# Kernel tuning notes

Hardware: AMD Instinct MI355X
Metric: run time of the kernel (lower is better)

The kernel has to match this reference:

```python
import jax, jax.numpy as jnp
import numpy as np

T, B, E, H = 2048, 4, 1024, 16
EH = E // H  # 64


def setup_inputs() -> dict:
    rng = jax.random.key(0)
    ks = jax.random.split(rng, 8)
    s = 0.02  # weight init scale to keep softmax logits reasonable
    return {
        "query": jax.random.normal(ks[0], (T, B, E), jnp.float32),
        "key": jax.random.normal(ks[1], (T, B, E), jnp.float32),
        "value": jax.random.normal(ks[2], (T, B, E), jnp.float32),
        "mask": jax.random.uniform(ks[3], (T, T), jnp.float32),
        "w_qkv": jax.random.normal(ks[4], (3 * E, E), jnp.float32) * s,
        "b_qkv": jax.random.normal(ks[5], (3 * E,), jnp.float32) * s,
        "w_out": jax.random.normal(ks[6], (E, E), jnp.float32) * s,
        "b_out": jax.random.normal(ks[7], (E,), jnp.float32) * s,
    }


def reference(query, key, value, mask, w_qkv, b_qkv, w_out, b_out):
    # query/key/value: [T, B, E] (sequence-first, as in the torch module)
    t, b, e = query.shape
    eh = e // H
    wq, wk, wv = jnp.split(w_qkv, 3, axis=0)  # each [E, E]
    bq, bk, bv = jnp.split(b_qkv, 3, axis=0)

    def proj_heads(x, w, bias):
        y = x @ w.T + bias                    # [T, B, E]
        # [T,B,H,Eh] -> [B,H,T,Eh]  (matches unflatten/transpose/permute chain)
        return y.reshape(t, b, H, eh).transpose(1, 2, 0, 3)

    q = proj_heads(query, wq, bq)             # [B, H, T, Eh]
    k = proj_heads(key, wk, bk)
    v = proj_heads(value, wv, bv)

    scale = 1.0 / np.sqrt(eh).astype(np.float32)
    scores = jnp.einsum('bhqd,bhkd->bhqk', q, k) * scale   # [B,H,T,T]
    scores = scores * mask[None, None, :, :]               # multiplicative mask
    # is_causal=False, attn_mask=None -> attn_bias is zeros (skip identity add)
    attn = jax.nn.softmax(scores, axis=-1)
    # dropout=0.0 -> identity
    ctx = jnp.einsum('bhqk,bhkd->bhqd', attn, v)           # [B,H,T,Eh]
    ctx = ctx.transpose(0, 2, 1, 3).reshape(b, t, e)       # [B,T,E]
    out = ctx @ w_out.T + b_out                            # [B,T,E]
    return out.transpose(1, 0, 2)                          # [T,B,E]
```

## Files before the change

kernel.cpp:

```cpp
#include <hip/hip_runtime.h>
#include <hip/hip_bf16.h>
#include <stdint.h>

#define T_DIM 2048
#define B_DIM 4
#define E_DIM 1024
#define H_DIM 16
#define EHD 64
#define L2E 1.4426950408889634f
#define QSCALE (0.125f * L2E)
#define FMAXC 12.0f

typedef __attribute__((ext_vector_type(8))) short bf16x8;
typedef __attribute__((ext_vector_type(4))) float f32x4;
typedef __attribute__((ext_vector_type(16))) float f32x16;
typedef __attribute__((ext_vector_type(2))) float f32x2;
typedef __attribute__((ext_vector_type(2))) unsigned u32x2;
typedef __attribute__((ext_vector_type(4))) unsigned u32x4;

__device__ __forceinline__ unsigned short f2bf(float x) {
  unsigned int u = __builtin_bit_cast(unsigned int, x);
  u += 0x7fffu + ((u >> 16) & 1u);
  return (unsigned short)(u >> 16);
}

__device__ __forceinline__ unsigned pkbf(float a, float b) {
  return (unsigned)f2bf(a) | ((unsigned)f2bf(b) << 16);
}

__device__ __forceinline__ unsigned pk_trunc(float a, float b) {
  return (__builtin_bit_cast(unsigned, a) >> 16) |
         (__builtin_bit_cast(unsigned, b) & 0xffff0000u);
}

__device__ __forceinline__ f32x2 bfpair1(unsigned w) {
  u32x2 u = {w << 16, w & 0xffff0000u};
  return __builtin_bit_cast(f32x2, u);
}

__device__ __forceinline__ void gload16(const void* g, void* l) {
  __builtin_amdgcn_global_load_lds(
      (const __attribute__((address_space(1))) void*)g,
      (__attribute__((address_space(3))) void*)l, 16, 0, 0);
}

__global__ __launch_bounds__(256) void cvt_fused(
    const float4* __restrict__ q, const float4* __restrict__ k,
    const float4* __restrict__ v, const float4* __restrict__ wqkv,
    const float4* __restrict__ wout, uint2* __restrict__ xq,
    uint2* __restrict__ xk, uint2* __restrict__ xv, uint2* __restrict__ wq,
    uint2* __restrict__ wo) {
  int i = blockIdx.x * 256 + threadIdx.x;
  const int stride = gridDim.x * 256;
  for (; i < 7340032; i += stride) {
    const float4* s;
    uint2* d;
    int j;
    if (i < 2097152) { s = q; d = xq; j = i; }
    else if (i < 4194304) { s = k; d = xk; j = i - 2097152; }
    else if (i < 6291456) { s = v; d = xv; j = i - 4194304; }
    else if (i < 7077888) { s = wqkv; d = wq; j = i - 6291456; }
    else { s = wout; d = wo; j = i - 7077888; }
    const float4 f = s[j];
    uint2 o;
    o.x = pkbf(f.x, f.y);
    o.y = pkbf(f.z, f.w);
    d[j] = o;
  }
}

__global__ __launch_bounds__(256) void mask_perm(const float* __restrict__ mask,
                                                 uint2* __restrict__ out) {
  const int idx = blockIdx.x * 256 + threadIdx.x;
  const int q = idx >> 8;
  const int k = (idx & 255) * 8;
  const float4 a = *(const float4*)(mask + (size_t)q * T_DIM + k);
  const float4 b = *(const float4*)(mask + (size_t)q * T_DIM + k + 4);
  const int qblk = q >> 7, wave = (q >> 5) & 3, ql = q & 31;
  const int t = k >> 6, kb = (k >> 5) & 1, half = (k >> 4) & 1;
  const int rem8 = (k >> 3) & 1;
  const int cbase = ((((qblk * 32 + t) * 4 + wave) * 2 + kb) * 2 + half) * 64;
  uint2 w0, w1;
  w0.x = pkbf(a.x, a.y);
  w0.y = pkbf(a.z, a.w);
  w1.x = pkbf(b.x, b.y);
  w1.y = pkbf(b.z, b.w);
  out[(size_t)(cbase + ql) * 2 + rem8] = w0;
  out[(size_t)(cbase + 32 + ql) * 2 + rem8] = w1;
}

template <int MODE>
__global__ __launch_bounds__(256) void gemm_kernel(
    const unsigned short* __restrict__ Abase,
    const unsigned short* __restrict__ Bt,
    const float* __restrict__ bias,
    void* __restrict__ outv, int K) {
  __shared__ alignas(16) short As[128 * 32];
  __shared__ alignas(16) short Bs[128 * 32];
  const int tid = threadIdx.x;
  const int lane = tid & 63, wave = tid >> 6;
  const int m0 = blockIdx.x * 128, n0 = blockIdx.y * 128;
  const int wr = wave >> 1, wc = wave & 1;
  const int lrow = lane & 15, lgrp = lane >> 4;

  const unsigned short* A = Abase;
  if (MODE == 0) A += (size_t)(n0 >> 10) * (8192u * 1024u);

  f32x4 acc[4][4];
#pragma unroll
  for (int m = 0; m < 4; ++m)
#pragma unroll
    for (int n = 0; n < 4; ++n) acc[m][n] = (f32x4){0.f, 0.f, 0.f, 0.f};

  const int srow = wave * 16 + (lane >> 2);
  const int scol = (lane & 3) * 8;
  short* lA0 = As + wave * 16 * 32;
  short* lA1 = As + (64 + wave * 16) * 32;
  short* lB0 = Bs + wave * 16 * 32;
  short* lB1 = Bs + (64 + wave * 16) * 32;

  for (int k0 = 0; k0 < K; k0 += 32) {
    const unsigned short* ga = A + (size_t)(m0 + srow) * K + k0 + scol;
    const unsigned short* gb = Bt + (size_t)(n0 + srow) * K + k0 + scol;
    gload16(ga, lA0);
    gload16(ga + (size_t)64 * K, lA1);
    gload16(gb, lB0);
    gload16(gb + (size_t)64 * K, lB1);
    __syncthreads();
    const short* pa = As + (wr * 64 + lrow) * 32 + lgrp * 8;
    const short* pb = Bs + (wc * 64 + lrow) * 32 + lgrp * 8;
    bf16x8 a[4], b[4];
#pragma unroll
    for (int m = 0; m < 4; ++m) a[m] = *(const bf16x8*)(pa + m * 512);
#pragma unroll
    for (int n = 0; n < 4; ++n) b[n] = *(const bf16x8*)(pb + n * 512);
#pragma unroll
    for (int m = 0; m < 4; ++m)
#pragma unroll
      for (int n = 0; n < 4; ++n)
        acc[m][n] = __builtin_amdgcn_mfma_f32_16x16x32_bf16(a[m], b[n], acc[m][n], 0, 0, 0);
    __syncthreads();
  }

#pragma unroll
  for (int n = 0; n < 4; ++n) {
    const int gn = n0 + wc * 64 + n * 16 + lrow;
    const float bv = bias[gn];
    if (MODE == 0) {
      unsigned short* out = (unsigned short*)outv;
      const int which = gn >> 10;
      const float qsc = (which == 0) ? QSCALE : 1.0f;
      const int e = gn & 1023;
      const int hh = e >> 6, dd = e & 63;
#pragma unroll
      for (int m = 0; m < 4; ++m)
#pragma unroll
        for (int r = 0; r < 4; ++r) {
          const int gm = m0 + wr * 64 + m * 16 + lgrp * 4 + r;
          const int t = gm >> 2, bb = gm & 3;
          const unsigned short val = f2bf((acc[m][n][r] + bv) * qsc);
          const size_t rbase = ((size_t)which * 64 + bb * 16 + hh) * 131072;
          if (which == 0) {
            out[rbase + (size_t)t * 64 + dd] = val;
          } else if (which == 1) {
            out[rbase + (t >> 6) * 4096 +
                (((t >> 5) & 1) * 4 + (dd >> 4)) * 512 +
                ((((dd >> 3) & 1) << 5) + (t & 31)) * 8 + (dd & 7)] = val;
          } else {
            out[rbase + (t >> 6) * 4096 +
                ((dd >> 5) * 4 + ((t >> 4) & 3)) * 512 +
                ((((t >> 3) & 1) << 5) + (dd & 31)) * 8 + (t & 7)] = val;
          }
        }
    } else {
      float* out = (float*)outv;
#pragma unroll
      for (int m = 0; m < 4; ++m)
#pragma unroll
        for (int r = 0; r < 4; ++r) {
          const int gm = m0 + wr * 64 + m * 16 + lgrp * 4 + r;
          const int bb = gm >> 11, t = gm & 2047;
          out[((size_t)t * B_DIM + bb) * E_DIM + gn] = acc[m][n][r] + bv;
        }
    }
  }
}

__global__ __launch_bounds__(256, 3) void attn_kernel(
    const unsigned short* __restrict__ Qm, const unsigned short* __restrict__ KPg,
    const unsigned short* __restrict__ VPg, const unsigned short* __restrict__ Mb,
    unsigned short* __restrict__ ctx) {
  __shared__ alignas(16) short Ks[2][4096];
  __shared__ alignas(16) short Vs[2][4096];
  const int tid = threadIdx.x, lane = tid & 63, wave = tid >> 6;
  const int ql = lane & 31, hi = lane >> 5;
  const int bh = blockIdx.y, b = bh >> 4, h = bh & 15;
  const int q0 = blockIdx.x * 128;
  const int qrow = q0 + wave * 32 + ql;

  const size_t base = (size_t)bh * (T_DIM * EHD);
  const uint4* mb4 = (const uint4*)Mb + (size_t)blockIdx.x * 32768 +
                     wave * 256 + lane;

  bf16x8 qf[4];
#pragma unroll
  for (int i = 0; i < 4; ++i)
    qf[i] = *(const bf16x8*)(Qm + base + (size_t)qrow * 64 + i * 16 + hi * 8);

  f32x16 accO0 = {0.f, 0.f, 0.f, 0.f, 0.f, 0.f, 0.f, 0.f,
                  0.f, 0.f, 0.f, 0.f, 0.f, 0.f, 0.f, 0.f};
  f32x16 accO1 = accO0;
  f32x2 racc2 = {0.f, 0.f};

  uint4 mreg[2][4];

#define STAGE(bufi, T_)                                                         \
  {                                                                             \
    _Pragma("unroll") for (int s2 = 0; s2 < 2; ++s2) {                          \
      const int s = wave * 2 + s2;                                              \
      gload16(KPg + base + (size_t)(T_) * 4096 + s * 512 + lane * 8,            \
              &Ks[bufi][s * 512]);                                              \
      gload16(VPg + base + (size_t)(T_) * 4096 + s * 512 + lane * 8,            \
              &Vs[bufi][s * 512]);                                              \
    }                                                                           \
    _Pragma("unroll") for (int u = 0; u < 4; ++u) {                             \
      mreg[bufi][u] = mb4[(size_t)(T_) * 1024 + u * 64];                        \
    }                                                                           \
  }

#define SOFTW(ACC, KB, HALF, W, MW)                                             \
  {                                                                             \
    const f32x2 mm = bfpair1(MW);                                               \
    const f32x2 sv = {ACC[HALF * 8 + 2 * W], ACC[HALF * 8 + 2 * W + 1]};        \
    const f32x2 tt =                                                            \
        __builtin_elementwise_fma(sv, mm, (f32x2){-FMAXC, -FMAXC});             \
    const float p0 = __builtin_amdgcn_exp2f(tt.x);                              \
    const float p1 = __builtin_amdgcn_exp2f(tt.y);                              \
    racc2 += (f32x2){p0, p1};                                                   \
    wk[KB][HALF * 4 + W] = pk_trunc(p0, p1);                                    \
  }

#define SOFTHALF(ACC, KB, HALF, MU)                                             \
  SOFTW(ACC, KB, HALF, 0, (MU).x)                                               \
  SOFTW(ACC, KB, HALF, 1, (MU).y)                                               \
  SOFTW(ACC, KB, HALF, 2, (MU).z)                                               \
  SOFTW(ACC, KB, HALF, 3, (MU).w)

#define PVCHUNK(KB, HF)                                                         \
  {                                                                             \
    unsigned a0 = wk[KB][HF * 4 + 0], a1 = wk[KB][HF * 4 + 1];                  \
    unsigned a2 = wk[KB][HF * 4 + 2], a3 = wk[KB][HF * 4 + 3];                  \
    asm("v_permlane32_swap_b32 %0, %1" : "+v"(a0), "+v"(a2));                   \
    asm("v_permlane32_swap_b32 %0, %1" : "+v"(a1), "+v"(a3));                   \
    const u32x4 pw = {a0, a1, a2, a3};                                          \
    const bf16x8 pa = __builtin_bit_cast(bf16x8, pw);                           \
    const bf16x8 vf0 =                                                          \
        *(const bf16x8*)(vb + (0 + (KB)*2 + (HF)) * 512 + lane * 8);            \
    const bf16x8 vf1 =                                                          \
        *(const bf16x8*)(vb + (4 + (KB)*2 + (HF)) * 512 + lane * 8);            \
    accO0 = __builtin_amdgcn_mfma_f32_32x32x16_bf16(vf0, pa, accO0, 0, 0, 0);   \
    accO1 = __builtin_amdgcn_mfma_f32_32x32x16_bf16(vf1, pa, accO1, 0, 0, 0);   \
  }

#define ATTN_ITER(CUR, DO_PRE, TN)                                              \
  {                                                                             \
    if (DO_PRE) {                                                               \
      STAGE((CUR) ^ 1, TN);                                                     \
      __builtin_amdgcn_sched_barrier(0);                                        \
    }                                                                           \
    const short* kbl = Ks[CUR];                                                 \
    const short* vb = Vs[CUR];                                                  \
    f32x16 accS0 = {0.f, 0.f, 0.f, 0.f, 0.f, 0.f, 0.f, 0.f,                     \
                    0.f, 0.f, 0.f, 0.f, 0.f, 0.f, 0.f, 0.f};                    \
    f32x16 accS1 = accS0;                                                       \
    __builtin_amdgcn_s_setprio(1);                                              \
    _Pragma("unroll") for (int i = 0; i < 4; ++i) {                             \
      const bf16x8 kf = *(const bf16x8*)(kbl + i * 512 + lane * 8);             \
      accS0 = __builtin_amdgcn_mfma_f32_32x32x16_bf16(kf, qf[i], accS0, 0, 0, 0); \
    }                                                                           \
    _Pragma("unroll") for (int i = 0; i < 4; ++i) {                             \
      const bf16x8 kf = *(const bf16x8*)(kbl + (4 + i) * 512 + lane * 8);       \
      accS1 = __builtin_amdgcn_mfma_f32_32x32x16_bf16(kf, qf[i], accS1, 0, 0, 0); \
    }                                                                           \
    __builtin_amdgcn_s_setprio(0);                                              \
    unsigned wk[2][8];                                                          \
    SOFTHALF(accS0, 0, 0, mreg[CUR][0])                                         \
    SOFTHALF(accS0, 0, 1, mreg[CUR][1])                                         \
    SOFTHALF(accS1, 1, 0, mreg[CUR][2])                                         \
    SOFTHALF(accS1, 1, 1, mreg[CUR][3])                                         \
    __builtin_amdgcn_s_setprio(1);                                              \
    PVCHUNK(0, 0)                                                               \
    PVCHUNK(0, 1)                                                               \
    PVCHUNK(1, 0)                                                               \
    PVCHUNK(1, 1)                                                               \
    __builtin_amdgcn_s_setprio(0);                                              \
  }

#define WAITBAR                                                                 \
  asm volatile("s_waitcnt vmcnt(0)" ::: "memory");                              \
  __builtin_amdgcn_sched_barrier(0);                                            \
  __builtin_amdgcn_s_barrier();                                                 \
  __builtin_amdgcn_sched_barrier(0);

  STAGE(0, 0);
  WAITBAR

  for (int tt = 0; tt < 15; ++tt) {
    ATTN_ITER(0, 1, 2 * tt + 1);
    WAITBAR
    ATTN_ITER(1, 1, 2 * tt + 2);
    WAITBAR
  }
  ATTN_ITER(0, 1, 31);
  WAITBAR
  ATTN_ITER(1, 0, 0);

#undef ATTN_ITER
#undef WAITBAR
#undef STAGE
#undef PVCHUNK
#undef SOFTHALF
#undef SOFTW

  float racc = racc2.x + racc2.y;
  racc += __shfl_xor(racc, 32);
  const float inv = 1.f / racc;
  unsigned short* cp =
      ctx + ((size_t)b * T_DIM + qrow) * E_DIM + h * 64 + hi * 4;
#define EPI(ACC, DBLK)                                                          \
  _Pragma("unroll") for (int rg = 0; rg < 4; ++rg) {                            \
    uint2 w;                                                                    \
    w.x = pkbf(ACC[rg * 4 + 0] * inv, ACC[rg * 4 + 1] * inv);                   \
    w.y = pkbf(ACC[rg * 4 + 2] * inv, ACC[rg * 4 + 3] * inv);                   \
    *(uint2*)(cp + (DBLK)*32 + rg * 8) = w;                                     \
  }
  EPI(accO0, 0)
  EPI(accO1, 1)
#undef EPI
}

extern "C" void kernel_launch(void* const* d_in, const int* in_sizes, int n_in,
                              void* d_out, int out_size, void* d_ws, size_t ws_size,
                              hipStream_t stream) {
  const float* q    = (const float*)d_in[0];
  const float* k    = (const float*)d_in[1];
  const float* v    = (const float*)d_in[2];
  const float* mask = (const float*)d_in[3];
  const float* wqkv = (const float*)d_in[4];
  const float* bqkv = (const float*)d_in[5];
  const float* wout = (const float*)d_in[6];
  const float* bout = (const float*)d_in[7];

  char* ws = (char*)d_ws;
  unsigned short* Xb   = (unsigned short*)(ws);
  unsigned short* Wqb  = (unsigned short*)(ws + 50331648);
  unsigned short* Wob  = (unsigned short*)(ws + 56623104);
  unsigned short* QKVb = (unsigned short*)(ws + 58720256);
  unsigned short* CTXb = (unsigned short*)(ws);
  unsigned short* Mb   = (unsigned short*)(ws + 16777216);

  cvt_fused<<<2048, 256, 0, stream>>>(
      (const float4*)q, (const float4*)k, (const float4*)v,
      (const float4*)wqkv, (const float4*)wout, (uint2*)Xb,
      (uint2*)(Xb + 8388608), (uint2*)(Xb + 16777216), (uint2*)Wqb,
      (uint2*)Wob);

  gemm_kernel<0><<<dim3(64, 24), 256, 0, stream>>>(Xb, Wqb, bqkv, QKVb, 1024);
  mask_perm<<<2048, 256, 0, stream>>>(mask, (uint2*)Mb);
  attn_kernel<<<dim3(16, 64), 256, 0, stream>>>(QKVb, QKVb + 8388608,
                                                QKVb + 16777216, Mb, CTXb);
  gemm_kernel<1><<<dim3(64, 8), 256, 0, stream>>>(CTXb, Wob, bout, d_out, 1024);
}
```

Before: 258.5 us.

## Widen GEMM K-tile to 64 with XOR-swizzled LDS and relax attention waitcnt

The projection GEMM now stages 64-wide K slices per iteration, with an XOR swizzle on the LDS column groups, and issues two MFMA sub-steps per barrier pair. This halves the number of barriers and load phases and is meant to cut LDS bank conflicts on the fragment reads. In the attention kernel a sched_barrier fixes the mask register loads after the K/V LDS loads, and the wait before the barrier drops from vmcnt(0) to vmcnt(4). The mask loads can then stay in flight across the barrier, but this relies on the exact order in which loads are issued for correctness.

```diff
diff --git a/kernel.cpp b/kernel.cpp
--- a/kernel.cpp
+++ b/kernel.cpp
@@ -95,8 +95,8 @@
     const unsigned short* __restrict__ Bt,
     const float* __restrict__ bias,
     void* __restrict__ outv, int K) {
-  __shared__ alignas(16) short As[128 * 32];
-  __shared__ alignas(16) short Bs[128 * 32];
+  __shared__ alignas(16) short As[128 * 64];
+  __shared__ alignas(16) short Bs[128 * 64];
   const int tid = threadIdx.x;
   const int lane = tid & 63, wave = tid >> 6;
   const int m0 = blockIdx.x * 128, n0 = blockIdx.y * 128;
@@ -112,33 +112,35 @@
 #pragma unroll
     for (int n = 0; n < 4; ++n) acc[m][n] = (f32x4){0.f, 0.f, 0.f, 0.f};
 
-  const int srow = wave * 16 + (lane >> 2);
-  const int scol = (lane & 3) * 8;
-  short* lA0 = As + wave * 16 * 32;
-  short* lA1 = As + (64 + wave * 16) * 32;
-  short* lB0 = Bs + wave * 16 * 32;
-  short* lB1 = Bs + (64 + wave * 16) * 32;
-
-  for (int k0 = 0; k0 < K; k0 += 32) {
-    const unsigned short* ga = A + (size_t)(m0 + srow) * K + k0 + scol;
-    const unsigned short* gb = Bt + (size_t)(n0 + srow) * K + k0 + scol;
-    gload16(ga, lA0);
-    gload16(ga + (size_t)64 * K, lA1);
-    gload16(gb, lB0);
-    gload16(gb + (size_t)64 * K, lB1);
+  const int rr8 = lane >> 3;
+  const int gc8 = ((lane & 7) ^ rr8) * 8;
+  const int rsw = lrow & 7;
+
+  for (int k0 = 0; k0 < K; k0 += 64) {
+#pragma unroll
+    for (int i = 0; i < 4; ++i) {
+      const int row = i * 32 + wave * 8;
+      gload16(A + (size_t)(m0 + row + rr8) * K + k0 + gc8, &As[row * 64]);
+      gload16(Bt + (size_t)(n0 + row + rr8) * K + k0 + gc8, &Bs[row * 64]);
+    }
     __syncthreads();
-    const short* pa = As + (wr * 64 + lrow) * 32 + lgrp * 8;
-    const short* pb = Bs + (wc * 64 + lrow) * 32 + lgrp * 8;
-    bf16x8 a[4], b[4];
-#pragma unroll
-    for (int m = 0; m < 4; ++m) a[m] = *(const bf16x8*)(pa + m * 512);
-#pragma unroll
-    for (int n = 0; n < 4; ++n) b[n] = *(const bf16x8*)(pb + n * 512);
-#pragma unroll
-    for (int m = 0; m < 4; ++m)
-#pragma unroll
-      for (int n = 0; n < 4; ++n)
-        acc[m][n] = __builtin_amdgcn_mfma_f32_16x16x32_bf16(a[m], b[n], acc[m][n], 0, 0, 0);
+#pragma unroll
+    for (int kk = 0; kk < 2; ++kk) {
+      const int cg = (((kk * 4 + lgrp) ^ rsw)) * 8;
+      const short* pa = As + (wr * 64 + lrow) * 64 + cg;
+      const short* pb = Bs + (wc * 64 + lrow) * 64 + cg;
+      bf16x8 a[4], b[4];
+#pragma unroll
+      for (int m = 0; m < 4; ++m) a[m] = *(const bf16x8*)(pa + m * 1024);
+#pragma unroll
+      for (int n = 0; n < 4; ++n) b[n] = *(const bf16x8*)(pb + n * 1024);
+#pragma unroll
+      for (int m = 0; m < 4; ++m)
+#pragma unroll
+        for (int n = 0; n < 4; ++n)
+          acc[m][n] =
+              __builtin_amdgcn_mfma_f32_16x16x32_bf16(a[m], b[n], acc[m][n], 0, 0, 0);
+    }
     __syncthreads();
   }
 
@@ -223,6 +225,7 @@
       gload16(VPg + base + (size_t)(T_) * 4096 + s * 512 + lane * 8,            \
               &Vs[bufi][s * 512]);                                              \
     }                                                                           \
+    __builtin_amdgcn_sched_barrier(0);                                          \
     _Pragma("unroll") for (int u = 0; u < 4; ++u) {                             \
       mreg[bufi][u] = mb4[(size_t)(T_) * 1024 + u * 64];                        \
     }                                                                           \
@@ -297,7 +300,7 @@
   }
 
 #define WAITBAR                                                                 \
-  asm volatile("s_waitcnt vmcnt(0)" ::: "memory");                              \
+  asm volatile("s_waitcnt vmcnt(4)" ::: "memory");                              \
   __builtin_amdgcn_sched_barrier(0);                                            \
   __builtin_amdgcn_s_barrier();                                                 \
   __builtin_amdgcn_sched_barrier(0);
```

After: 239.2 us (median of 2 runs). -7.5%, faster.
